# Performance work log

Measured on AMD Instinct MI355X. Metric: run time of the kernel, lower is better.

## Reference

```python
import jax, jax.numpy as jnp
import numpy as np

N_EMBD = 1024
N_HEADS = 16
HEAD_SIZE = N_EMBD // N_HEADS
BLOCK_SIZE = 2048
BATCH = 2
SEQ = 2048
EPS = 1e-5


def setup_inputs() -> dict:
    key = jax.random.key(0)
    ks = jax.random.split(key, 12)
    s = 0.02
    x = jax.random.normal(ks[0], (BATCH, SEQ, N_EMBD), dtype=jnp.float32)
    # per-head Q/K/V weights concatenated: [n_embd, n_heads*head_size]
    Wq = jax.random.normal(ks[1], (N_EMBD, N_EMBD), dtype=jnp.float32) * s
    Wk = jax.random.normal(ks[2], (N_EMBD, N_EMBD), dtype=jnp.float32) * s
    Wv = jax.random.normal(ks[3], (N_EMBD, N_EMBD), dtype=jnp.float32) * s
    Wproj = jax.random.normal(ks[4], (N_EMBD, N_EMBD), dtype=jnp.float32) * s
    bproj = jnp.zeros((N_EMBD,), dtype=jnp.float32)
    W1 = jax.random.normal(ks[5], (N_EMBD, 4 * N_EMBD), dtype=jnp.float32) * s
    b1 = jnp.zeros((4 * N_EMBD,), dtype=jnp.float32)
    W2 = jax.random.normal(ks[6], (4 * N_EMBD, N_EMBD), dtype=jnp.float32) * s
    b2 = jnp.zeros((N_EMBD,), dtype=jnp.float32)
    ln1_w = jnp.ones((N_EMBD,), dtype=jnp.float32)
    ln1_b = jnp.zeros((N_EMBD,), dtype=jnp.float32)
    ln2_w = jnp.ones((N_EMBD,), dtype=jnp.float32)
    ln2_b = jnp.zeros((N_EMBD,), dtype=jnp.float32)
    return dict(x=x, Wq=Wq, Wk=Wk, Wv=Wv, Wproj=Wproj, bproj=bproj,
                W1=W1, b1=b1, W2=W2, b2=b2,
                ln1_w=ln1_w, ln1_b=ln1_b, ln2_w=ln2_w, ln2_b=ln2_b)


def _layer_norm(x, w, b):
    mu = jnp.mean(x, axis=-1, keepdims=True)
    var = jnp.var(x, axis=-1, keepdims=True)
    return (x - mu) * jax.lax.rsqrt(var + EPS) * w + b


def reference(x, Wq, Wk, Wv, Wproj, bproj, W1, b1, W2, b2, ln1_w, ln1_b, ln2_w, ln2_b):
    B, T, C = x.shape
    # --- attention sub-block (pre-LN) ---
    h = _layer_norm(x, ln1_w, ln1_b)
    # project then split heads: [B,T,H,D] -> [B,H,T,D]
    def split(W):
        return (h @ W).reshape(B, T, N_HEADS, HEAD_SIZE).transpose(0, 2, 1, 3)
    q, k, v = split(Wq), split(Wk), split(Wv)
    # NOTE: original code scales by C**-0.5 with C = n_embd (not head_size)
    scores = jnp.einsum('bhtd,bhsd->bhts', q, k) * (C ** -0.5)  # [B,H,T,T]
    causal = jnp.tril(jnp.ones((T, T), dtype=bool))
    scores = jnp.where(causal, scores, -jnp.inf)
    wei = jax.nn.softmax(scores, axis=-1)
    attn = jnp.einsum('bhts,bhsd->bhtd', wei, v)  # [B,H,T,D]
    attn = attn.transpose(0, 2, 1, 3).reshape(B, T, C)  # concat heads
    x = x + attn @ Wproj + bproj
    # --- FFN sub-block (pre-LN) ---
    h2 = _layer_norm(x, ln2_w, ln2_b)
    ff = jax.nn.relu(h2 @ W1 + b1) @ W2 + b2
    return x + ff
```

## Files before the change

### kernel.cpp

```cpp
#include <hip/hip_runtime.h>
#include <cstdint>

typedef __attribute__((ext_vector_type(8))) __bf16 bf16_8;
typedef __attribute__((ext_vector_type(4))) __bf16 bf16_4;
typedef __attribute__((ext_vector_type(4))) float f32x4;

#define QSCALE 0.045084220027780106f

__device__ __forceinline__ void gld_lds16(const __bf16* g, __bf16* l) {
  __builtin_amdgcn_global_load_lds(
      (const __attribute__((address_space(1))) void*)(void*)g,
      (__attribute__((address_space(3))) void*)l, 16, 0, 0);
}

__global__ __launch_bounds__(256) void convt_k(
    const float* __restrict__ Wq, const float* __restrict__ Wk,
    const float* __restrict__ Wv, const float* __restrict__ Wp,
    const float* __restrict__ W1, const float* __restrict__ W2,
    __bf16* __restrict__ WqT, __bf16* __restrict__ WkT,
    __bf16* __restrict__ WvT, __bf16* __restrict__ WpT,
    __bf16* __restrict__ W1T, __bf16* __restrict__ W2T) {
  int bid = blockIdx.x;
  const float* in; __bf16* outp; int Kd, Nd, tile;
  if (bid < 4096) {
    int m = bid >> 10; tile = bid & 1023; Kd = 1024; Nd = 1024;
    in   = m == 0 ? Wq  : m == 1 ? Wk  : m == 2 ? Wv  : Wp;
    outp = m == 0 ? WqT : m == 1 ? WkT : m == 2 ? WvT : WpT;
  } else if (bid < 8192) {
    tile = bid - 4096; Kd = 1024; Nd = 4096; in = W1; outp = W1T;
  } else {
    tile = bid - 8192; Kd = 4096; Nd = 1024; in = W2; outp = W2T;
  }
  int tilesN = Nd >> 5;
  int tk = tile / tilesN, tn = tile % tilesN;
  int k0 = tk * 32, n0 = tn * 32;
  __shared__ float tbuf[32][33];
  int tx = threadIdx.x & 31, ty = threadIdx.x >> 5;
#pragma unroll
  for (int i = 0; i < 4; ++i)
    tbuf[ty + i * 8][tx] = in[(size_t)(k0 + ty + i * 8) * Nd + (n0 + tx)];
  __syncthreads();
#pragma unroll
  for (int i = 0; i < 4; ++i)
    outp[(size_t)(n0 + ty + i * 8) * Kd + (k0 + tx)] = (__bf16)tbuf[tx][ty + i * 8];
}

__global__ __launch_bounds__(256) void ln_k(const float* __restrict__ x,
                                            const float* __restrict__ w,
                                            const float* __restrict__ b,
                                            __bf16* __restrict__ out) {
  int row = blockIdx.x;
  int tid = threadIdx.x;
  f32x4 v = *(const f32x4*)(x + (size_t)row * 1024 + tid * 4);
  float s = v[0] + v[1] + v[2] + v[3];
  float sq = v[0] * v[0] + v[1] * v[1] + v[2] * v[2] + v[3] * v[3];
#pragma unroll
  for (int m = 1; m < 64; m <<= 1) { s += __shfl_xor(s, m); sq += __shfl_xor(sq, m); }
  __shared__ float rs[4], rq[4];
  int wave = tid >> 6, lane = tid & 63;
  if (lane == 0) { rs[wave] = s; rq[wave] = sq; }
  __syncthreads();
  s  = rs[0] + rs[1] + rs[2] + rs[3];
  sq = rq[0] + rq[1] + rq[2] + rq[3];
  float mu   = s * (1.f / 1024.f);
  float var  = sq * (1.f / 1024.f) - mu * mu;
  float rstd = rsqrtf(var + 1e-5f);
  f32x4 wv = *(const f32x4*)(w + tid * 4);
  f32x4 bv = *(const f32x4*)(b + tid * 4);
  bf16_4 o;
#pragma unroll
  for (int i = 0; i < 4; ++i) o[i] = (__bf16)((v[i] - mu) * rstd * wv[i] + bv[i]);
  *(bf16_4*)(out + (size_t)row * 1024 + tid * 4) = o;
}

template <int MODE, int BM, int BN>
__global__ __launch_bounds__(256) void gemm_k(
    const __bf16* __restrict__ A,
    const __bf16* __restrict__ B0, const __bf16* __restrict__ B1,
    const __bf16* __restrict__ B2,
    __bf16* __restrict__ O0, __bf16* __restrict__ O1, __bf16* __restrict__ O2,
    float* __restrict__ Of,
    const float* __restrict__ bias, const float* __restrict__ res,
    int K, int Nchunk, int nBlkM, int nBlkN) {
  constexpr int MT = BM / 32, NT = BN / 32;
  __shared__ __align__(16) __bf16 As[BM * 32];
  __shared__ __align__(16) __bf16 Bs[BN * 32];
  int chunk = blockIdx.y;
  const __bf16* Bt = chunk == 0 ? B0 : (chunk == 1 ? B1 : B2);
  __bf16* Ob       = chunk == 0 ? O0 : (chunk == 1 ? O1 : O2);
  int pid = blockIdx.x;
  const int GM = 8;
  int perG = GM * nBlkN;
  int gid = pid / perG;
  int fm = gid * GM;
  int gsz = min(nBlkM - fm, GM);
  int bm = fm + (pid % gsz);
  int bn = (pid % perG) / gsz;
  int m0 = bm * BM, n0 = bn * BN;
  int tid = threadIdx.x, wave = tid >> 6, lane = tid & 63;
  int quad = lane >> 4, l16 = lane & 15;
  int wm = (wave & 1) * (BM / 2), wn = (wave >> 1) * (BN / 2);

  f32x4 z = {0.f, 0.f, 0.f, 0.f};
  f32x4 acc[MT][NT];
#pragma unroll
  for (int mt = 0; mt < MT; ++mt)
#pragma unroll
    for (int nt = 0; nt < NT; ++nt) acc[mt][nt] = z;

  const __bf16* Ag = A  + (size_t)m0 * K;
  const __bf16* Bg = Bt + (size_t)n0 * K;
  int srow = lane >> 2;
  int scol = (lane & 3) * 8;

  for (int k0 = 0; k0 < K; k0 += 32) {
#pragma unroll
    for (int i = 0; i < BM / 64; ++i) {
      int row = i * 64 + wave * 16 + srow;
      gld_lds16(Ag + (size_t)row * K + k0 + scol, As + (i * 64 + wave * 16) * 32);
    }
#pragma unroll
    for (int i = 0; i < BN / 64; ++i) {
      int row = i * 64 + wave * 16 + srow;
      gld_lds16(Bg + (size_t)row * K + k0 + scol, Bs + (i * 64 + wave * 16) * 32);
    }
    __syncthreads();
    bf16_8 af[MT], bfr[NT];
#pragma unroll
    for (int t = 0; t < MT; ++t)
      af[t] = *(const bf16_8*)(As + (wm + t * 16 + l16) * 32 + quad * 8);
#pragma unroll
    for (int t = 0; t < NT; ++t)
      bfr[t] = *(const bf16_8*)(Bs + (wn + t * 16 + l16) * 32 + quad * 8);
#pragma unroll
    for (int mt = 0; mt < MT; ++mt)
#pragma unroll
      for (int nt = 0; nt < NT; ++nt)
        acc[mt][nt] = __builtin_amdgcn_mfma_f32_16x16x32_bf16(af[mt], bfr[nt],
                                                              acc[mt][nt], 0, 0, 0);
    __syncthreads();
  }

  if (MODE == 0 && chunk == 2) {
#pragma unroll
    for (int mt = 0; mt < MT; ++mt) {
      int mbase = m0 + wm + mt * 16 + quad * 4;
      int bb = mbase >> 11, tt = mbase & 2047;
#pragma unroll
      for (int nt = 0; nt < NT; ++nt) {
        int n = n0 + wn + nt * 16 + l16;
        bf16_4 pk;
#pragma unroll
        for (int r = 0; r < 4; ++r) pk[r] = (__bf16)acc[mt][nt][r];
        *(bf16_4*)(O2 + ((size_t)((bb * 16 + (n >> 6)) * 64 + (n & 63))) * 2048 + tt) = pk;
      }
    }
    return;
  }

  float oscale = (MODE == 0 && chunk == 0) ? QSCALE : 1.0f;
#pragma unroll
  for (int mt = 0; mt < MT; ++mt) {
#pragma unroll
    for (int r = 0; r < 4; ++r) {
      int m = m0 + wm + mt * 16 + quad * 4 + r;
      size_t rowo = (size_t)m * Nchunk;
#pragma unroll
      for (int nt = 0; nt < NT; ++nt) {
        int n = n0 + wn + nt * 16 + l16;
        float v = acc[mt][nt][r];
        if (MODE == 0) {
          Ob[rowo + n] = (__bf16)(v * oscale);
        } else if (MODE == 1) {
          v += bias[n]; v = v > 0.f ? v : 0.f;
          Ob[rowo + n] = (__bf16)v;
        } else {
          v += bias[n] + res[rowo + n];
          Of[rowo + n] = v;
        }
      }
    }
  }
}

__global__ __launch_bounds__(256) void attn_k(const __bf16* __restrict__ Q,
                                              const __bf16* __restrict__ K,
                                              const __bf16* __restrict__ Vt,
                                              __bf16* __restrict__ O) {
  __shared__ __align__(16) __bf16 Kls[2][64 * 64];
  __shared__ __align__(16) __bf16 Vls[2][64 * 64];
  __shared__ __align__(16) __bf16 Pls[4][16 * 72];

  int blk = blockIdx.x;
  int qt = blk & 31, bh = blk >> 5;
  int h = bh & 15, b = bh >> 4;
  int q0 = qt * 64;
  int tid = threadIdx.x, wave = tid >> 6, lane = tid & 63;
  int quad = lane >> 4, l16 = lane & 15;
  int qw = q0 + wave * 16;
  int qrow = qw + l16;
  int r8 = lane >> 3, c8 = lane & 7;
  int cswz = c8 ^ r8;
  int so0 = (quad ^ (l16 & 7)) * 8;
  int so1 = so0 ^ 32;

  const __bf16* Qg = Q + ((size_t)(b * 2048 + qw + l16)) * 1024 + h * 64;
  bf16_8 qf0 = *(const bf16_8*)(Qg + quad * 8);
  bf16_8 qf1 = *(const bf16_8*)(Qg + 32 + quad * 8);

  const __bf16* Kb = K + (size_t)(b * 2048) * 1024 + h * 64;
  const __bf16* Vh = Vt + (size_t)((b * 16 + h) * 64) * 2048;

  f32x4 z = {0.f, 0.f, 0.f, 0.f};
  f32x4 ot[4];
#pragma unroll
  for (int dt = 0; dt < 4; ++dt) ot[dt] = z;
  float l_acc = 0.f;
  __bf16* Pw = &Pls[wave][0];

  auto stage = [&](int kt, int buf) {
#pragma unroll
    for (int i = 0; i < 2; ++i) {
      int rl = wave * 16 + i * 8 + r8;
      gld_lds16(Kb + (size_t)(kt + rl) * 1024 + cswz * 8,
                &Kls[buf][(wave * 16 + i * 8) * 64]);
      gld_lds16(Vh + (size_t)rl * 2048 + kt + cswz * 8,
                &Vls[buf][(wave * 16 + i * 8) * 64]);
    }
  };

  auto body = [&](int kt, int buf, bool masked) {
    f32x4 sf[4];
#pragma unroll
    for (int kk = 0; kk < 4; ++kk) {
      const __bf16* kr = &Kls[buf][(kk * 16 + l16) * 64];
      bf16_8 ka = *(const bf16_8*)(kr + so0);
      bf16_8 kb = *(const bf16_8*)(kr + so1);
      f32x4 a = z;
      a = __builtin_amdgcn_mfma_f32_16x16x32_bf16(ka, qf0, a, 0, 0, 0);
      a = __builtin_amdgcn_mfma_f32_16x16x32_bf16(kb, qf1, a, 0, 0, 0);
      sf[kk] = a;
    }
#pragma unroll
    for (int kk = 0; kk < 4; ++kk) {
      bf16_4 pk;
#pragma unroll
      for (int r = 0; r < 4; ++r) {
        float x = sf[kk][r];
        if (masked && (kt + kk * 16 + quad * 4 + r > qrow)) x = -1e30f;
        float p = __builtin_amdgcn_exp2f(x);
        l_acc += p;
        pk[r] = (__bf16)p;
      }
      *(bf16_4*)(Pw + l16 * 72 + kk * 16 + quad * 4) = pk;
    }
    bf16_8 pf0 = *(const bf16_8*)(Pw + l16 * 72 + quad * 8);
    bf16_8 pf1 = *(const bf16_8*)(Pw + l16 * 72 + 32 + quad * 8);
#pragma unroll
    for (int dt = 0; dt < 4; ++dt) {
      const __bf16* vr = &Vls[buf][(dt * 16 + l16) * 64];
      bf16_8 v0 = *(const bf16_8*)(vr + so0);
      bf16_8 v1 = *(const bf16_8*)(vr + so1);
      ot[dt] = __builtin_amdgcn_mfma_f32_16x16x32_bf16(v0, pf0, ot[dt], 0, 0, 0);
      ot[dt] = __builtin_amdgcn_mfma_f32_16x16x32_bf16(v1, pf1, ot[dt], 0, 0, 0);
    }
  };

  stage(0, 0);
  __syncthreads();
  int cur = 0;
  for (int it = 0; it < qt; ++it) {
    stage((it + 1) * 64, cur ^ 1);
    body(it * 64, cur, false);
    __syncthreads();
    cur ^= 1;
  }
  body(qt * 64, cur, true);

  float l = l_acc;
  l += __shfl_xor(l, 16);
  l += __shfl_xor(l, 32);
  float inv = 1.0f / l;
  size_t base = (size_t)(b * 2048 + qw + l16) * 1024 + h * 64;
#pragma unroll
  for (int dt = 0; dt < 4; ++dt) {
    bf16_4 ok;
#pragma unroll
    for (int r = 0; r < 4; ++r) ok[r] = (__bf16)(ot[dt][r] * inv);
    *(bf16_4*)(O + base + dt * 16 + quad * 4) = ok;
  }
}

extern "C" void kernel_launch(void* const* d_in, const int* in_sizes, int n_in,
                              void* d_out, int out_size, void* d_ws,
                              size_t ws_size, hipStream_t stream) {
  const float* x   = (const float*)d_in[0];
  const float* Wq  = (const float*)d_in[1];
  const float* Wk  = (const float*)d_in[2];
  const float* Wv  = (const float*)d_in[3];
  const float* Wp  = (const float*)d_in[4];
  const float* bp  = (const float*)d_in[5];
  const float* W1  = (const float*)d_in[6];
  const float* b1  = (const float*)d_in[7];
  const float* W2  = (const float*)d_in[8];
  const float* b2  = (const float*)d_in[9];
  const float* l1w = (const float*)d_in[10];
  const float* l1b = (const float*)d_in[11];
  const float* l2w = (const float*)d_in[12];
  const float* l2b = (const float*)d_in[13];
  float* out = (float*)d_out;
  char* ws = (char*)d_ws;
  const size_t MB = 1024ull * 1024ull;
  __bf16* WqT = (__bf16*)(ws + 0 * MB);
  __bf16* WkT = (__bf16*)(ws + 2 * MB);
  __bf16* WvT = (__bf16*)(ws + 4 * MB);
  __bf16* WpT = (__bf16*)(ws + 6 * MB);
  __bf16* W1T = (__bf16*)(ws + 8 * MB);
  __bf16* W2T = (__bf16*)(ws + 16 * MB);
  __bf16* hb  = (__bf16*)(ws + 24 * MB);
  __bf16* Qb  = (__bf16*)(ws + 32 * MB);
  __bf16* Kb_ = (__bf16*)(ws + 40 * MB);
  __bf16* Vt  = (__bf16*)(ws + 48 * MB);
  __bf16* Ab  = (__bf16*)(ws + 56 * MB);
  __bf16* F1  = (__bf16*)(ws + 64 * MB);

  convt_k<<<12288, 256, 0, stream>>>(Wq, Wk, Wv, Wp, W1, W2,
                                     WqT, WkT, WvT, WpT, W1T, W2T);
  ln_k<<<4096, 256, 0, stream>>>(x, l1w, l1b, hb);
  gemm_k<0, 128, 128><<<dim3(256, 3), 256, 0, stream>>>(
      hb, WqT, WkT, WvT, Qb, Kb_, Vt, nullptr, nullptr, nullptr,
      1024, 1024, 32, 8);
  attn_k<<<1024, 256, 0, stream>>>(Qb, Kb_, Vt, Ab);
  gemm_k<2, 128, 64><<<dim3(512, 1), 256, 0, stream>>>(
      Ab, WpT, WpT, WpT, nullptr, nullptr, nullptr, out, bp, x,
      1024, 1024, 32, 16);
  ln_k<<<4096, 256, 0, stream>>>(out, l2w, l2b, hb);
  gemm_k<1, 128, 128><<<dim3(1024, 1), 256, 0, stream>>>(
      hb, W1T, W1T, W1T, F1, F1, F1, nullptr, b1, nullptr,
      1024, 4096, 32, 32);
  gemm_k<2, 128, 64><<<dim3(512, 1), 256, 0, stream>>>(
      F1, W2T, W2T, W2T, nullptr, nullptr, nullptr, out, b2, out,
      4096, 1024, 32, 16);
}
```

Before: 399.3 us.

## Double-buffer GEMM LDS tiles with XOR swizzle and retile N=1024 GEMMs

The GEMM kernel now keeps two LDS buffers so the next K-slice's global-to-LDS loads are issued before the current slice is computed, which removes one barrier per iteration. The LDS layout gets an XOR swizzle on 16-byte chunks to reduce bank conflicts. A BK template parameter is added, and the projection and FFN2 GEMMs switch to 64x64 tiles with BK=64 to launch more blocks. The extra LDS use may lower occupancy, and the smaller tiles reuse less data.

```diff
diff --git a/kernel.cpp b/kernel.cpp
--- a/kernel.cpp
+++ b/kernel.cpp
@@ -73,7 +73,7 @@
   *(bf16_4*)(out + (size_t)row * 1024 + tid * 4) = o;
 }
 
-template <int MODE, int BM, int BN>
+template <int MODE, int BM, int BN, int BK>
 __global__ __launch_bounds__(256) void gemm_k(
     const __bf16* __restrict__ A,
     const __bf16* __restrict__ B0, const __bf16* __restrict__ B1,
@@ -82,9 +82,14 @@
     float* __restrict__ Of,
     const float* __restrict__ bias, const float* __restrict__ res,
     int K, int Nchunk, int nBlkM, int nBlkN) {
+  constexpr int NC = BK / 8;
   constexpr int MT = BM / 32, NT = BN / 32;
-  __shared__ __align__(16) __bf16 As[BM * 32];
-  __shared__ __align__(16) __bf16 Bs[BN * 32];
+  constexpr int KK = BK / 32;
+  constexpr int RPC = 64 / NC;
+  constexpr int CA = BM / RPC / 4;
+  constexpr int CB = BN / RPC / 4;
+  __shared__ __align__(16) __bf16 As[2][BM * BK];
+  __shared__ __align__(16) __bf16 Bs[2][BN * BK];
   int chunk = blockIdx.y;
   const __bf16* Bt = chunk == 0 ? B0 : (chunk == 1 ? B1 : B2);
   __bf16* Ob       = chunk == 0 ? O0 : (chunk == 1 ? O1 : O2);
@@ -100,6 +105,7 @@
   int tid = threadIdx.x, wave = tid >> 6, lane = tid & 63;
   int quad = lane >> 4, l16 = lane & 15;
   int wm = (wave & 1) * (BM / 2), wn = (wave >> 1) * (BN / 2);
+  int srow = lane / NC, schunk = lane % NC;
 
   f32x4 z = {0.f, 0.f, 0.f, 0.f};
   f32x4 acc[MT][NT];
@@ -110,36 +116,56 @@
 
   const __bf16* Ag = A  + (size_t)m0 * K;
   const __bf16* Bg = Bt + (size_t)n0 * K;
-  int srow = lane >> 2;
-  int scol = (lane & 3) * 8;
-
-  for (int k0 = 0; k0 < K; k0 += 32) {
-#pragma unroll
-    for (int i = 0; i < BM / 64; ++i) {
-      int row = i * 64 + wave * 16 + srow;
-      gld_lds16(Ag + (size_t)row * K + k0 + scol, As + (i * 64 + wave * 16) * 32);
-    }
-#pragma unroll
-    for (int i = 0; i < BN / 64; ++i) {
-      int row = i * 64 + wave * 16 + srow;
-      gld_lds16(Bg + (size_t)row * K + k0 + scol, Bs + (i * 64 + wave * 16) * 32);
-    }
+
+  auto stage = [&](int k0, int buf) {
+#pragma unroll
+    for (int i = 0; i < CA; ++i) {
+      int r0 = (wave * CA + i) * RPC;
+      int gc = schunk ^ ((r0 + srow) & (NC - 1));
+      gld_lds16(Ag + (size_t)(r0 + srow) * K + k0 + gc * 8, &As[buf][r0 * BK]);
+    }
+#pragma unroll
+    for (int i = 0; i < CB; ++i) {
+      int r0 = (wave * CB + i) * RPC;
+      int gc = schunk ^ ((r0 + srow) & (NC - 1));
+      gld_lds16(Bg + (size_t)(r0 + srow) * K + k0 + gc * 8, &Bs[buf][r0 * BK]);
+    }
+  };
+
+  auto compute = [&](int buf) {
+#pragma unroll
+    for (int kk = 0; kk < KK; ++kk) {
+      bf16_8 af[MT], bfr[NT];
+#pragma unroll
+      for (int t = 0; t < MT; ++t) {
+        int r = wm + t * 16 + l16;
+        int lc = (kk * 4 + quad) ^ (r & (NC - 1));
+        af[t] = *(const bf16_8*)(&As[buf][r * BK + lc * 8]);
+      }
+#pragma unroll
+      for (int t = 0; t < NT; ++t) {
+        int r = wn + t * 16 + l16;
+        int lc = (kk * 4 + quad) ^ (r & (NC - 1));
+        bfr[t] = *(const bf16_8*)(&Bs[buf][r * BK + lc * 8]);
+      }
+#pragma unroll
+      for (int mt = 0; mt < MT; ++mt)
+#pragma unroll
+        for (int nt = 0; nt < NT; ++nt)
+          acc[mt][nt] = __builtin_amdgcn_mfma_f32_16x16x32_bf16(af[mt], bfr[nt],
+                                                                acc[mt][nt], 0, 0, 0);
+    }
+  };
+
+  int niter = K / BK;
+  stage(0, 0);
+  __syncthreads();
+  for (int it = 0; it < niter - 1; ++it) {
+    stage((it + 1) * BK, (it + 1) & 1);
+    compute(it & 1);
     __syncthreads();
-    bf16_8 af[MT], bfr[NT];
-#pragma unroll
-    for (int t = 0; t < MT; ++t)
-      af[t] = *(const bf16_8*)(As + (wm + t * 16 + l16) * 32 + quad * 8);
-#pragma unroll
-    for (int t = 0; t < NT; ++t)
-      bfr[t] = *(const bf16_8*)(Bs + (wn + t * 16 + l16) * 32 + quad * 8);
-#pragma unroll
-    for (int mt = 0; mt < MT; ++mt)
-#pragma unroll
-      for (int nt = 0; nt < NT; ++nt)
-        acc[mt][nt] = __builtin_amdgcn_mfma_f32_16x16x32_bf16(af[mt], bfr[nt],
-                                                              acc[mt][nt], 0, 0, 0);
-    __syncthreads();
-  }
+  }
+  compute((niter - 1) & 1);
 
   if (MODE == 0 && chunk == 2) {
 #pragma unroll
@@ -327,18 +353,18 @@
   convt_k<<<12288, 256, 0, stream>>>(Wq, Wk, Wv, Wp, W1, W2,
                                      WqT, WkT, WvT, WpT, W1T, W2T);
   ln_k<<<4096, 256, 0, stream>>>(x, l1w, l1b, hb);
-  gemm_k<0, 128, 128><<<dim3(256, 3), 256, 0, stream>>>(
+  gemm_k<0, 128, 128, 32><<<dim3(256, 3), 256, 0, stream>>>(
       hb, WqT, WkT, WvT, Qb, Kb_, Vt, nullptr, nullptr, nullptr,
       1024, 1024, 32, 8);
   attn_k<<<1024, 256, 0, stream>>>(Qb, Kb_, Vt, Ab);
-  gemm_k<2, 128, 64><<<dim3(512, 1), 256, 0, stream>>>(
+  gemm_k<2, 64, 64, 64><<<dim3(1024, 1), 256, 0, stream>>>(
       Ab, WpT, WpT, WpT, nullptr, nullptr, nullptr, out, bp, x,
-      1024, 1024, 32, 16);
+      1024, 1024, 64, 16);
   ln_k<<<4096, 256, 0, stream>>>(out, l2w, l2b, hb);
-  gemm_k<1, 128, 128><<<dim3(1024, 1), 256, 0, stream>>>(
+  gemm_k<1, 128, 128, 32><<<dim3(1024, 1), 256, 0, stream>>>(
       hb, W1T, W1T, W1T, F1, F1, F1, nullptr, b1, nullptr,
       1024, 4096, 32, 32);
-  gemm_k<2, 128, 64><<<dim3(512, 1), 256, 0, stream>>>(
+  gemm_k<2, 64, 64, 64><<<dim3(1024, 1), 256, 0, stream>>>(
       F1, W2T, W2T, W2T, nullptr, nullptr, nullptr, out, b2, out,
-      4096, 1024, 32, 16);
-}
+      4096, 1024, 64, 16);
+}
```

Measured after the change: 356.8 us. -10.7%, faster.
